# Kernel tuning notes

Hardware: AMD Instinct MI355X
Metric: run time of the kernel (lower is better)

## Reference

```python
import jax, jax.numpy as jnp
import numpy as np
from math import sqrt

B, S, E, H = 2, 2048, 768, 12
DH = E // H
W = 256            # one-sided attention window (attention_window=512)
G = 16             # number of global tokens (positions 0..G-1 in every batch row)
PAD = 128          # last PAD tokens per row are padding (masked)
FF = 3072          # SwiGLU intermediate size
NEG = -1e9
EPS = 1e-5


def _ln(x, g, b):
    m = jnp.mean(x, axis=-1, keepdims=True)
    v = jnp.var(x, axis=-1, keepdims=True)
    return (x - m) * jax.lax.rsqrt(v + EPS) * g + b


def _rope(x, t):
    # x: [B,H,S,DH]; t: [B,S] float 'set positions'
    half = DH // 2
    inv_freq = 1.0 / (10000.0 ** (jnp.arange(half, dtype=jnp.float32) / half))
    ang = t[:, None, :, None] * inv_freq            # [B,1,S,half]
    cos, sin = jnp.cos(ang), jnp.sin(ang)
    x1, x2 = x[..., :half], x[..., half:]
    return jnp.concatenate([x1 * cos - x2 * sin, x2 * cos + x1 * sin], axis=-1)


def _heads(x):  # [B,S,E] -> [B,H,S,DH]
    return x.reshape(B, S, H, DH).transpose(0, 2, 1, 3)


def _chunk3(x):
    # [B,H,S,D] -> [B,H,C,3W,D]: for query chunk c, keys from chunks c-1,c,c+1 (zero padded)
    b, h, s, d = x.shape
    c = s // W
    xp = jnp.pad(x, ((0, 0), (0, 0), (W, W), (0, 0))).reshape(b, h, c + 2, W, d)
    return jnp.concatenate([xp[:, :, :-2], xp[:, :, 1:-1], xp[:, :, 2:]], axis=3)


def _forward(x, attention_mask, global_attention_mask,
             Wq, bq, Wk, bk, Wv, bv, Wqg, bqg, Wkg, bkg, Wvg, bvg,
             ln0_g, ln0_b, ln1_g, ln1_b, W1, W3, W2):
    C = S // W
    merged = attention_mask * (global_attention_mask + 1)   # 0 masked, 1 local, 2 global
    is_masked = merged == 0
    is_global = merged == 2
    remove = merged != 1   # keys removed from windowed attention (masked or global)

    q = _heads(x @ Wq + bq) / sqrt(DH)
    k = _heads(x @ Wk + bk)
    v = _heads(x @ Wv + bv)

    # RoPE over 'set positions': (~is_index_masked) * cumsum(is_index_global_attn)
    t = jnp.where(is_masked, 0, jnp.cumsum(is_global.astype(jnp.int32), axis=1)).astype(jnp.float32)
    q = _rope(q, t)
    k = _rope(k, t)

    # --- sliding-window (banded) scores: band[b,h,i,d] = q_i . k_{i+d-W} ---
    qc = q.reshape(B, H, C, W, DH)
    k3 = _chunk3(k)
    s3 = jnp.einsum('bhcpd,bhcqd->bhcpq', qc, k3)                     # [B,H,C,W,3W]
    didx = jnp.arange(W)[:, None] + jnp.arange(2 * W + 1)[None, :]    # [W,2W+1]
    band = jnp.take_along_axis(s3, didx[None, None, None], axis=-1)   # [B,H,C,W,2W+1]

    # mask removed keys / out-of-range positions inside the band
    rmp = jnp.pad(remove, ((0, 0), (W, W)), constant_values=True).reshape(B, C + 2, W)
    rm3 = jnp.concatenate([rmp[:, :-2], rmp[:, 1:-1], rmp[:, 2:]], axis=2)  # [B,C,3W]
    band_rm = jnp.take_along_axis(jnp.broadcast_to(rm3[:, :, None, :], (B, C, W, 3 * W)),
                                  didx[None, None], axis=-1)                # [B,C,W,2W+1]
    band = jnp.where(band_rm[:, None], NEG, band).reshape(B, H, S, 2 * W + 1)

    # --- global-key columns (keys taken from the RoPE'd local key vectors) ---
    sg = jnp.einsum('bhid,bhgd->bhig', q, k[:, :, :G])                # [B,H,S,G]

    scores = jnp.concatenate([sg, band], axis=-1)                     # [B,H,S,G+2W+1]
    probs = jax.nn.softmax(scores.astype(jnp.float32), axis=-1).astype(x.dtype)
    probs = jnp.where(is_masked[:, None, :, None], 0.0, probs)

    # --- probs @ value: global columns + band ---
    out = jnp.einsum('bhig,bhgd->bhid', probs[..., :G], v[:, :, :G])
    pl = probs[..., G:].reshape(B, H, C, W, 2 * W + 1)
    rows = jnp.broadcast_to(jnp.arange(W)[:, None], (W, 2 * W + 1))
    p3 = jnp.zeros((B, H, C, W, 3 * W), probs.dtype).at[:, :, :, rows, didx].set(pl)
    v3 = _chunk3(v)
    out = out + jnp.einsum('bhcpq,bhcqd->bhcpd', p3, v3).reshape(B, H, S, DH)
    attn = out.transpose(0, 2, 1, 3).reshape(B, S, E)

    # --- full attention for global tokens (separate global projections, no RoPE) ---
    gq = _heads(x @ Wqg + bqg)[:, :, :G] / sqrt(DH)                   # [B,H,G,DH]
    gk = _heads(x @ Wkg + bkg)
    gv = _heads(x @ Wvg + bvg)
    gs = jnp.einsum('bhgd,bhjd->bhgj', gq, gk)                        # [B,H,G,S]
    gs = jnp.where(is_masked[:, None, None, :], NEG, gs)
    gp = jax.nn.softmax(gs.astype(jnp.float32), axis=-1).astype(x.dtype)
    gout = jnp.einsum('bhgj,bhjd->bhgd', gp, gv).transpose(0, 2, 1, 3).reshape(B, G, E)
    attn = attn.at[:, :G].set(gout)

    # residual + post-LN, SwiGLU FFN, residual + post-LN (dropout = eval mode)
    h0 = _ln(x + attn, ln0_g, ln0_b)
    ffn = (jax.nn.silu(h0 @ W1) * (h0 @ W3)) @ W2
    return _ln(h0 + ffn, ln1_g, ln1_b)


def setup_inputs():
    key = jax.random.key(0)
    ks = jax.random.split(key, 12)
    x = jax.random.normal(ks[0], (B, S, E), jnp.float32)
    attention_mask = jnp.ones((B, S), jnp.int32).at[:, S - PAD:].set(0)
    global_attention_mask = jnp.zeros((B, S), jnp.int32).at[:, :G].set(1)
    sd = 0.02
    def w(k, shape):
        return jax.random.normal(k, shape, jnp.float32) * sd
    return dict(
        x=x, attention_mask=attention_mask, global_attention_mask=global_attention_mask,
        Wq=w(ks[1], (E, E)), bq=jnp.zeros((E,), jnp.float32),
        Wk=w(ks[2], (E, E)), bk=jnp.zeros((E,), jnp.float32),
        Wv=w(ks[3], (E, E)), bv=jnp.zeros((E,), jnp.float32),
        Wqg=w(ks[4], (E, E)), bqg=jnp.zeros((E,), jnp.float32),
        Wkg=w(ks[5], (E, E)), bkg=jnp.zeros((E,), jnp.float32),
        Wvg=w(ks[6], (E, E)), bvg=jnp.zeros((E,), jnp.float32),
        ln0_g=jnp.ones((E,), jnp.float32), ln0_b=jnp.zeros((E,), jnp.float32),
        ln1_g=jnp.ones((E,), jnp.float32), ln1_b=jnp.zeros((E,), jnp.float32),
        W1=w(ks[7], (E, FF)), W3=w(ks[8], (E, FF)), W2=w(ks[9], (FF, E)))


def reference(x, attention_mask, global_attention_mask, Wq, bq, Wk, bk, Wv, bv,
              Wqg, bqg, Wkg, bkg, Wvg, bvg, ln0_g, ln0_b, ln1_g, ln1_b, W1, W3, W2):
    return _forward(x, attention_mask, global_attention_mask,
                    Wq, bq, Wk, bk, Wv, bv, Wqg, bqg, Wkg, bkg, Wvg, bvg,
                    ln0_g, ln0_b, ln1_g, ln1_b, W1, W3, W2)
```

## Files before the change

kernel.cpp:

```cpp
#include <hip/hip_runtime.h>


#define BB_ 2
#define SS 2048
#define EE 768
#define HH 12
#define DHH 64
#define GG 16
#define FFN 3072
#define MM (BB_*SS)

typedef __bf16 bf16_t;
typedef __bf16 bf16x8_t __attribute__((ext_vector_type(8)));
typedef float f32x4_t __attribute__((ext_vector_type(4)));

__device__ inline void gload16(const void* g, void* l) {
  __builtin_amdgcn_global_load_lds((const __attribute__((address_space(1))) void*)g,
                                   (__attribute__((address_space(3))) void*)l, 16, 0, 0);
}

__global__ __launch_bounds__(64) void detect_kernel(const unsigned int* __restrict__ w,
                                                    int* __restrict__ flag) {
  int cnt = 0;
  for (int i = threadIdx.x; i < 1024; i += 64) {
    unsigned e = (w[i] >> 7) & 0xFF;
    cnt += (e >= 100 && e <= 144) ? 1 : 0;
  }
  for (int off = 32; off; off >>= 1) cnt += __shfl_xor(cnt, off);
  if (threadIdx.x == 0) flag[0] = (cnt > 512) ? 1 : 0;
}

struct CanonP { const void* src[11]; bf16_t* dst[11]; };

__global__ __launch_bounds__(256) void canon_kernel(CanonP P, const int* __restrict__ flag) {
  constexpr int ns[11] = {3145728, 768,768,768,768,768,768, 768,768,768,768};
  int idx4 = (blockIdx.x*256 + threadIdx.x)*4;
  const bool isb = flag[0] != 0;
  int off = 0, seg = -1, loc = 0;
  #pragma unroll
  for (int i=0;i<11;i++) {
    if (seg < 0 && idx4 < off + ns[i]) { seg = i; loc = idx4 - off; }
    off += ns[i];
  }
  if (seg < 0) return;
  const void* s = P.src[seg];
  bf16_t* d = P.dst[seg];
  if (isb) {
    *(uint2*)&d[loc] = *(const uint2*)((const unsigned short*)s + loc);
  } else {
    float4 v = *(const float4*)((const float*)s + loc);
    d[loc+0] = (bf16_t)v.x; d[loc+1] = (bf16_t)v.y;
    d[loc+2] = (bf16_t)v.z; d[loc+3] = (bf16_t)v.w;
  }
}

struct TP6 { const void* s[6]; bf16_t* d[6]; };

__global__ __launch_bounds__(256) void trans_kernel(TP6 P, int R, int C,
                                                    const int* __restrict__ flag) {
  const int z = blockIdx.z;
  const void* src = P.s[z]; bf16_t* dst = P.d[z];
  const bool isb = flag[0] != 0;
  __shared__ bf16_t tile[32][33];
  int tx = threadIdx.x & 31, ty = threadIdx.x >> 5;
  int r0 = blockIdx.y*32, c0 = blockIdx.x*32;
  #pragma unroll
  for (int i=0;i<4;i++) {
    int rr = ty + i*8;
    size_t si = (size_t)(r0+rr)*C + c0 + tx;
    tile[rr][tx] = isb ? ((const bf16_t*)src)[si] : (bf16_t)((const float*)src)[si];
  }
  __syncthreads();
  #pragma unroll
  for (int i=0;i<4;i++) {
    int cc = ty + i*8;
    dst[(size_t)(c0+cc)*R + r0 + tx] = tile[tx][cc];
  }
}

__global__ __launch_bounds__(256) void zero_kernel(float* __restrict__ p, int n) {
  int i = blockIdx.x*256 + threadIdx.x;
  if (i < n) p[i] = 0.f;
}

__global__ __launch_bounds__(256) void flags_kernel(const int* __restrict__ am,
                                                    const int* __restrict__ gm,
                                                    float* __restrict__ tpos,
                                                    int* __restrict__ flags) {
  int b = blockIdx.x;
  int t = threadIdx.x;
  int lane = t & 63, wv = t >> 6;
  int base = b*SS + t*8;
  int mg[8]; int isg[8]; int loc = 0;
  for (int i=0;i<8;i++) {
    int a = am[base+i], g = gm[base+i];
    int merged = a*(g+1);
    mg[i] = merged;
    isg[i] = (merged==2) ? 1 : 0;
    loc += isg[i];
  }
  int x = loc;
  for (int off=1; off<64; off<<=1) {
    int y = __shfl_up(x, off);
    if (lane >= off) x += y;
  }
  __shared__ int wtot[4];
  if (lane==63) wtot[wv] = x;
  __syncthreads();
  int prev = 0;
  for (int w=0; w<wv; w++) prev += wtot[w];
  int run = prev + x - loc;
  for (int i=0;i<8;i++) {
    run += isg[i];
    int masked = (mg[i]==0) ? 1 : 0;
    int glob   = (mg[i]==2) ? 1 : 0;
    int rem    = (mg[i]!=1) ? 1 : 0;
    tpos[base+i]  = masked ? 0.f : (float)run;
    flags[base+i] = masked | (glob<<1) | (rem<<2);
  }
}

__device__ inline void gemm128_core(const bf16_t* __restrict__ A,
                                    const bf16_t* __restrict__ BT,
                                    int ldA, int ldB, int kbeg, int kend,
                                    int m0, int n0,
                                    bf16_t* As, bf16_t* Bs,
                                    f32x4_t (&acc)[4][4]) {
  const int t = threadIdx.x;
  const int lane = t & 63, wv = t >> 6;
  const int l15 = lane & 15, quad = lane >> 4;
  const int wr = (wv >> 1) << 6, wc = (wv & 1) << 6;
  const int rsub = lane >> 3, pch = lane & 7;
  const int sch = pch ^ rsub;
  const size_t abase = (size_t)(m0 + wv*32 + rsub)*ldA + sch*8;
  const size_t bbase = (size_t)(n0 + wv*32 + rsub)*ldB + sch*8;
  const int sx = l15 & 7;
  bf16_t* lA = As + (wv*32)*64;
  bf16_t* lB = Bs + (wv*32)*64;
  for (int k0 = kbeg; k0 < kend; k0 += 64) {
    __syncthreads();
    #pragma unroll
    for (int j=0;j<4;j++) {
      gload16(A + abase + (size_t)(j*8)*ldA + k0, lA + j*8*64);
      gload16(BT + bbase + (size_t)(j*8)*ldB + k0, lB + j*8*64);
    }
    __syncthreads();
    #pragma unroll
    for (int c=0;c<2;c++) {
      bf16x8_t af[4], bfr[4];
      #pragma unroll
      for (int a=0;a<4;a++)
        af[a] = *(const bf16x8_t*)&As[(wr + a*16 + l15)*64 + ((c*4+quad)^sx)*8];
      #pragma unroll
      for (int b=0;b<4;b++)
        bfr[b] = *(const bf16x8_t*)&Bs[(wc + b*16 + l15)*64 + ((c*4+quad)^sx)*8];
      #pragma unroll
      for (int a=0;a<4;a++)
        #pragma unroll
        for (int b=0;b<4;b++)
          acc[a][b] = __builtin_amdgcn_mfma_f32_16x16x32_bf16(af[a], bfr[b], acc[a][b], 0,0,0);
    }
  }
}

struct ProjParams {
  const bf16_t* W[5];
  const bf16_t* Bi[5];
  bf16_t* O[5];
};

__global__ __launch_bounds__(256) void proj_kernel(const bf16_t* __restrict__ x,
                                                   ProjParams P,
                                                   const float* __restrict__ tpos) {
  const int m0 = blockIdx.x*128, n0 = blockIdx.y*128;
  const int z  = blockIdx.z;
  __shared__ bf16_t As[128*64];
  __shared__ bf16_t Bs[128*64];
  f32x4_t acc[4][4];
  #pragma unroll
  for (int a=0;a<4;a++)
    #pragma unroll
    for (int b=0;b<4;b++) acc[a][b] = (f32x4_t){0.f,0.f,0.f,0.f};
  gemm128_core(x, P.W[z], EE, EE, 0, EE, m0, n0, As, Bs, acc);

  const int t = threadIdx.x;
  const int lane = t & 63, wv = t >> 6;
  const int l15 = lane & 15, quad = lane >> 4;
  const int wr = (wv >> 1) << 6, wc = (wv & 1) << 6;
  const float scale = (z==0) ? 0.125f : 1.f;
  const bool rope = (z<2);
  const int h = (n0 + wc) >> 6;
  bf16_t* Oz = P.O[z];
  const bf16_t* Bz = P.Bi[z];
  float bvals[4];
  #pragma unroll
  for (int b=0;b<4;b++) bvals[b] = (float)Bz[h*64 + b*16 + l15];
  #pragma unroll
  for (int a=0;a<4;a++) {
    #pragma unroll
    for (int r=0;r<4;r++) {
      int row = m0 + wr + a*16 + quad*4 + r;
      int bb = row >> 11, spos = row & (SS-1);
      float vals[4];
      #pragma unroll
      for (int b=0;b<4;b++) vals[b] = (acc[a][b][r] + bvals[b]) * scale;
      if (rope) {
        float tv = tpos[row];
        #pragma unroll
        for (int b=0;b<2;b++) {
          int j = b*16 + l15;
          float inv = __expf(-(float)j * (9.210340371976184f/32.f));
          float ang = tv * inv;
          float sn = __sinf(ang), cs = __cosf(ang);
          float x1 = vals[b], x2 = vals[b+2];
          vals[b]   = x1*cs - x2*sn;
          vals[b+2] = x2*cs + x1*sn;
        }
      }
      bf16_t* dst = Oz + ((size_t)(bb*HH + h)*SS + spos)*DHH;
      #pragma unroll
      for (int b=0;b<4;b++) dst[b*16 + l15] = (bf16_t)vals[b];
    }
  }
}

__global__ __launch_bounds__(256) void gemm_ffn1(const bf16_t* __restrict__ A,
                                                 const bf16_t* __restrict__ BT,
                                                 bf16_t* __restrict__ t1) {
  const int m0 = blockIdx.x*128, n0 = blockIdx.y*128;
  __shared__ bf16_t As[128*64];
  __shared__ bf16_t Bs[128*64];
  f32x4_t acc[4][4];
  #pragma unroll
  for (int a=0;a<4;a++)
    #pragma unroll
    for (int b=0;b<4;b++) acc[a][b] = (f32x4_t){0.f,0.f,0.f,0.f};
  gemm128_core(A, BT, EE, EE, 0, EE, m0, n0, As, Bs, acc);
  const int t = threadIdx.x;
  const int lane = t & 63, wv = t >> 6;
  const int l15 = lane & 15, quad = lane >> 4;
  const int wr = (wv >> 1) << 6, wc = (wv & 1) << 6;
  #pragma unroll
  for (int a=0;a<4;a++)
    #pragma unroll
    for (int r=0;r<4;r++) {
      int row = m0 + wr + a*16 + quad*4 + r;
      #pragma unroll
      for (int b=0;b<4;b++)
        t1[(size_t)row*FFN + n0 + wc + b*16 + l15] = (bf16_t)acc[a][b][r];
    }
}

__global__ __launch_bounds__(256) void gemm_ffn3(const bf16_t* __restrict__ A,
                                                 const bf16_t* __restrict__ BT,
                                                 const bf16_t* __restrict__ t1,
                                                 bf16_t* __restrict__ g1) {
  const int m0 = blockIdx.x*128, n0 = blockIdx.y*128;
  __shared__ bf16_t As[128*64];
  __shared__ bf16_t Bs[128*64];
  f32x4_t acc[4][4];
  #pragma unroll
  for (int a=0;a<4;a++)
    #pragma unroll
    for (int b=0;b<4;b++) acc[a][b] = (f32x4_t){0.f,0.f,0.f,0.f};
  gemm128_core(A, BT, EE, EE, 0, EE, m0, n0, As, Bs, acc);
  const int t = threadIdx.x;
  const int lane = t & 63, wv = t >> 6;
  const int l15 = lane & 15, quad = lane >> 4;
  const int wr = (wv >> 1) << 6, wc = (wv & 1) << 6;
  #pragma unroll
  for (int a=0;a<4;a++)
    #pragma unroll
    for (int r=0;r<4;r++) {
      int row = m0 + wr + a*16 + quad*4 + r;
      #pragma unroll
      for (int b=0;b<4;b++) {
        size_t idx = (size_t)row*FFN + n0 + wc + b*16 + l15;
        float a1 = (float)t1[idx];
        float sil = a1 / (1.f + __expf(-a1));
        g1[idx] = (bf16_t)(sil * acc[a][b][r]);
      }
    }
}

struct Ffn2Out { float* p[4]; };

__global__ __launch_bounds__(256) void gemm_ffn2(const bf16_t* __restrict__ A,
                                                 const bf16_t* __restrict__ BT,
                                                 Ffn2Out O) {
  const int m0 = blockIdx.x*128, n0 = blockIdx.y*128;
  const int kz = blockIdx.z;
  __shared__ bf16_t As[128*64];
  __shared__ bf16_t Bs[128*64];
  f32x4_t acc[4][4];
  #pragma unroll
  for (int a=0;a<4;a++)
    #pragma unroll
    for (int b=0;b<4;b++) acc[a][b] = (f32x4_t){0.f,0.f,0.f,0.f};
  gemm128_core(A, BT, FFN, FFN, kz*768, (kz+1)*768, m0, n0, As, Bs, acc);
  const int t = threadIdx.x;
  const int lane = t & 63, wv = t >> 6;
  const int l15 = lane & 15, quad = lane >> 4;
  const int wr = (wv >> 1) << 6, wc = (wv & 1) << 6;
  float* C = O.p[kz];
  #pragma unroll
  for (int a=0;a<4;a++)
    #pragma unroll
    for (int r=0;r<4;r++) {
      int row = m0 + wr + a*16 + quad*4 + r;
      #pragma unroll
      for (int b=0;b<4;b++)
        C[(size_t)row*EE + n0 + wc + b*16 + l15] = acc[a][b][r];
    }
}

__global__ __launch_bounds__(64) void qg_kernel(const bf16_t* __restrict__ x,
                                                const bf16_t* __restrict__ WqgT,
                                                const bf16_t* __restrict__ bqg,
                                                float* __restrict__ qgb) {
  int g = blockIdx.x, h = blockIdx.y, b = blockIdx.z;
  int d = threadIdx.x;
  __shared__ float xs[EE];
  for (int i=d; i<EE; i+=64) xs[i] = (float)x[((size_t)b*SS + g)*EE + i];
  __syncthreads();
  float acc = 0.f;
  const bf16_t* wrow = WqgT + (size_t)(h*64+d)*EE;
  #pragma unroll 4
  for (int k=0;k<EE;k+=8) {
    bf16x8_t w8 = *(const bf16x8_t*)(wrow + k);
    #pragma unroll
    for (int i=0;i<8;i++) acc += xs[k+i] * (float)w8[i];
  }
  acc = (acc + (float)bqg[h*64+d]) * 0.125f;
  qgb[((size_t)(b*HH+h)*GG + g)*DHH + d] = acc;
}

__global__ __launch_bounds__(256) void band_kernel(const bf16_t* __restrict__ qb,
                                                   const bf16_t* __restrict__ kb,
                                                   const bf16_t* __restrict__ vb,
                                                   const int* __restrict__ flags,
                                                   float* __restrict__ attn) {
  const int p0 = blockIdx.x*64;
  const int h = blockIdx.y, b = blockIdx.z;
  const int t = threadIdx.x;
  const int wv = t>>6, lane = t&63;
  const int l15 = lane & 15, quad = lane >> 4;
  const size_t bh = (size_t)(b*HH+h);
  const bf16_t* kbh = kb + bh*SS*DHH;
  const bf16_t* vbh = vb + bh*SS*DHH;
  const int* fl = flags + b*SS;
  const int q0 = p0 + wv*16;

  __shared__ bf16_t Vt[64*72];
  __shared__ bf16_t Pw[4][16*72];

  const bf16_t* qrow = qb + (bh*SS + q0 + l15)*DHH;
  bf16x8_t qa0 = *(const bf16x8_t*)(qrow + quad*8);
  bf16x8_t qa1 = *(const bf16x8_t*)(qrow + 32 + quad*8);

  f32x4_t o[4];
  #pragma unroll
  for (int i=0;i<4;i++) o[i] = (f32x4_t){0.f,0.f,0.f,0.f};
  float lsum[4] = {0.f,0.f,0.f,0.f};
  bf16_t* P = Pw[wv];

  for (int unit=0; unit<10; unit++) {
    const int kb0 = (unit<9) ? (p0 - 256 + unit*64) : 0;
    __syncthreads();
    {
      int kp  = (t & 31)*2;
      int dh0 = (t >> 5)*8;
      int k1 = kb0 + kp, k2 = kb0 + kp + 1;
      int kc1 = min(max(k1,0),SS-1), kc2 = min(max(k2,0),SS-1);
      bf16x8_t v1 = *(const bf16x8_t*)(vbh + (size_t)kc1*DHH + dh0);
      bf16x8_t v2 = *(const bf16x8_t*)(vbh + (size_t)kc2*DHH + dh0);
      #pragma unroll
      for (int i=0;i<8;i++) {
        union { unsigned u; bf16_t hh[2]; } pk;
        pk.hh[0] = v1[i]; pk.hh[1] = v2[i];
        *(unsigned*)&Vt[(dh0+i)*72 + kp] = pk.u;
      }
    }
    __syncthreads();
    const int nsub = (unit<9) ? 4 : 1;
    for (int sub=0; sub<4; sub++) {
      if (sub < nsub) {
        int kpos = kb0 + sub*16 + l15;
        int kc = min(max(kpos,0),SS-1);
        const bf16_t* krow = kbh + (size_t)kc*DHH;
        bf16x8_t kf0 = *(const bf16x8_t*)(krow + quad*8);
        bf16x8_t kf1 = *(const bf16x8_t*)(krow + 32 + quad*8);
        f32x4_t s = (f32x4_t){0.f,0.f,0.f,0.f};
        s = __builtin_amdgcn_mfma_f32_16x16x32_bf16(qa0, kf0, s, 0,0,0);
        s = __builtin_amdgcn_mfma_f32_16x16x32_bf16(qa1, kf1, s, 0,0,0);
        bool drop = false;
        if (unit<9) drop = (kpos<0) || (kpos>=SS) || (((fl[kc]>>2)&1)!=0);
        #pragma unroll
        for (int r=0;r<4;r++) {
          float e;
          if (unit==9) {
            e = __expf(s[r]);
          } else {
            int dj = kpos - (q0 + quad*4 + r);
            bool valid = (dj>=-256) && (dj<=256) && (!drop);
            e = valid ? __expf(s[r]) : 0.f;
          }
          lsum[r] += e;
          P[(quad*4+r)*72 + sub*16 + l15] = (bf16_t)e;
        }
      } else {
        #pragma unroll
        for (int r=0;r<4;r++) P[(quad*4+r)*72 + sub*16 + l15] = (bf16_t)0.f;
      }
    }
    #pragma unroll
    for (int chunk=0; chunk<2; chunk++) {
      bf16x8_t pf = *(const bf16x8_t*)&P[l15*72 + chunk*32 + quad*8];
      #pragma unroll
      for (int nt=0; nt<4; nt++) {
        bf16x8_t vf = *(const bf16x8_t*)&Vt[(nt*16+l15)*72 + chunk*32 + quad*8];
        o[nt] = __builtin_amdgcn_mfma_f32_16x16x32_bf16(pf, vf, o[nt], 0,0,0);
      }
    }
  }
  #pragma unroll
  for (int r=0;r<4;r++) {
    float s = lsum[r];
    s += __shfl_xor(s,1); s += __shfl_xor(s,2);
    s += __shfl_xor(s,4); s += __shfl_xor(s,8);
    lsum[r] = s;
  }
  #pragma unroll
  for (int r=0;r<4;r++) {
    int q = q0 + quad*4 + r;
    int masked = fl[q] & 1;
    float inv = masked ? 0.f : 1.f/lsum[r];
    float* dst = attn + ((size_t)(b*SS+q))*EE + h*64 + l15;
    #pragma unroll
    for (int nt=0; nt<4; nt++) dst[nt*16] = o[nt][r]*inv;
  }
}

__global__ __launch_bounds__(256) void gattn_part(const float* __restrict__ qgb,
                                                  const bf16_t* __restrict__ kgb,
                                                  const bf16_t* __restrict__ vgb,
                                                  const int* __restrict__ flags,
                                                  float* __restrict__ go,
                                                  float* __restrict__ gl) {
  const int kbase = blockIdx.x*128;
  const int h = blockIdx.y, b = blockIdx.z;
  const int t = threadIdx.x;
  __shared__ float gqs[16*68];
  __shared__ float Ks[64*68];
  __shared__ float Vs[64*68];
  __shared__ float es[16*64];
  const size_t bh = (size_t)(b*HH+h);
  #pragma unroll
  for (int j=0;j<4;j++) {
    int idx = t + j*256;
    int g = idx>>6, d = idx&63;
    gqs[g*68+d] = qgb[(bh*GG + g)*DHH + d];
  }
  float accv[4] = {0.f,0.f,0.f,0.f};
  float lpart = 0.f;
  const int gs = t>>4, kslot = t&15;
  const int dp = t&63, grp = t>>6;
  const bf16_t* kb_ = kgb + bh*SS*DHH;
  const bf16_t* vb_ = vgb + bh*SS*DHH;
  const int* fl = flags + b*SS;
  for (int tile=0; tile<2; tile++) {
    int k0 = kbase + tile*64;
    __syncthreads();
    {
      int row = t>>2, seg = t&3;
      const bf16_t* sk = kb_ + (size_t)(k0+row)*DHH + seg*16;
      const bf16_t* sv = vb_ + (size_t)(k0+row)*DHH + seg*16;
      bf16x8_t k1 = *(const bf16x8_t*)sk;
      bf16x8_t k2 = *(const bf16x8_t*)(sk+8);
      bf16x8_t v1 = *(const bf16x8_t*)sv;
      bf16x8_t v2 = *(const bf16x8_t*)(sv+8);
      #pragma unroll
      for (int i=0;i<8;i++) {
        Ks[row*68 + seg*16 + i]     = (float)k1[i];
        Ks[row*68 + seg*16 + 8 + i] = (float)k2[i];
        Vs[row*68 + seg*16 + i]     = (float)v1[i];
        Vs[row*68 + seg*16 + 8 + i] = (float)v2[i];
      }
    }
    __syncthreads();
    #pragma unroll
    for (int j=0;j<4;j++) {
      int key = kslot + 16*j;
      const float* gq = &gqs[gs*68];
      const float* kr = &Ks[key*68];
      float s = 0.f;
      #pragma unroll
      for (int d4=0; d4<64; d4+=4) {
        float4 a = *(const float4*)(gq + d4);
        float4 kk = *(const float4*)(kr + d4);
        s += a.x*kk.x + a.y*kk.y + a.z*kk.z + a.w*kk.w;
      }
      int msk = fl[k0+key] & 1;
      float e = msk ? 0.f : __expf(s);
      es[gs*64+key] = e;
      lpart += e;
    }
    __syncthreads();
    #pragma unroll
    for (int g=0; g<4; g++) {
      int gg = grp*4+g;
      float a = accv[g];
      for (int key=0;key<64;key++) a += es[gg*64+key]*Vs[key*68+dp];
      accv[g] = a;
    }
  }
  __syncthreads();
  es[gs*64 + kslot] = lpart;
  __syncthreads();
  if (t < 16) {
    float s = 0.f;
    for (int j=0;j<16;j++) s += es[t*64+j];
    atomicAdd(&gl[bh*16 + t], s);
  }
  #pragma unroll
  for (int g=0; g<4; g++)
    atomicAdd(&go[(bh*16 + grp*4+g)*64 + dp], accv[g]);
}

__global__ __launch_bounds__(256) void addln_kernel(const bf16_t* __restrict__ Abf,
                                                    const float* __restrict__ Af,
                                                    const float* __restrict__ B0,
                                                    const float* __restrict__ B1,
                                                    const float* __restrict__ B2,
                                                    const float* __restrict__ B3,
                                                    const float* __restrict__ gof,
                                                    const float* __restrict__ glf,
                                                    const bf16_t* __restrict__ gw,
                                                    const bf16_t* __restrict__ bw,
                                                    float* __restrict__ outf,
                                                    bf16_t* __restrict__ outb,
                                                    const int* __restrict__ flagp) {
  int r = blockIdx.x, t = threadIdx.x;
  int lane = t&63, wv = t>>6;
  int spos = r & (SS-1), bb = r >> 11;
  bool isglob = (gof != nullptr) && (spos < GG);
  float v[3]; float sum=0.f, ss=0.f;
  #pragma unroll
  for (int j=0;j<3;j++) {
    int idx = t + j*256;
    size_t gi = (size_t)r*EE+idx;
    float a = Abf ? (float)Abf[gi] : Af[gi];
    float bv;
    if (isglob) {
      int hh = idx >> 6, dp = idx & 63;
      int slot = (bb*HH + hh)*GG + spos;
      bv = gof[(size_t)slot*DHH + dp] / glf[slot];
    } else {
      bv = B0[gi];
    }
    float val = a + bv;
    if (B1) val += B1[gi] + B2[gi] + B3[gi];
    v[j] = val; sum += val; ss += val*val;
  }
  #pragma unroll
  for (int off=32; off>=1; off>>=1) {
    sum += __shfl_xor(sum, off);
    ss  += __shfl_xor(ss, off);
  }
  __shared__ float s1[4], s2[4];
  if (lane==0) { s1[wv]=sum; s2[wv]=ss; }
  __syncthreads();
  sum = s1[0]+s1[1]+s1[2]+s1[3];
  ss  = s2[0]+s2[1]+s2[2]+s2[3];
  float mean = sum * (1.f/(float)EE);
  float var  = ss * (1.f/(float)EE) - mean*mean;
  float rstd = rsqrtf(var + 1e-5f);
  bool wantb, wantf;
  if (flagp) { bool isb = (*flagp)!=0; wantb = isb; wantf = !isb; }
  else { wantb = (outb!=nullptr); wantf = (outf!=nullptr); }
  #pragma unroll
  for (int j=0;j<3;j++) {
    int idx = t + j*256;
    float o = (v[j]-mean)*rstd*(float)gw[idx] + (float)bw[idx];
    if (wantf) outf[(size_t)r*EE+idx] = o;
    if (wantb) outb[(size_t)r*EE+idx] = (bf16_t)o;
  }
}

extern "C" void kernel_launch(void* const* d_in, const int* in_sizes, int n_in,
                              void* d_out, int out_size, void* d_ws, size_t ws_size,
                              hipStream_t stream) {
  const void* x_r    = d_in[0];
  const int* am      = (const int*)d_in[1];
  const int* gm      = (const int*)d_in[2];
  (void)in_sizes; (void)n_in; (void)out_size; (void)ws_size;

  char* ws = (char*)d_ws;
  size_t off = 0;
  auto alloc = [&](size_t bytes) -> void* {
    void* p = ws + off;
    off += (bytes + 255) & ~(size_t)255;
    return p;
  };
  bf16_t* xc    = (bf16_t*)alloc((size_t)MM*EE*2);
  bf16_t* WT[6]; bf16_t* bc[6];
  for (int i=0;i<6;i++) { WT[i] = (bf16_t*)alloc((size_t)EE*EE*2); bc[i] = (bf16_t*)alloc(EE*2); }
  bf16_t* lnc[4];
  for (int i=0;i<4;i++) lnc[i] = (bf16_t*)alloc(EE*2);
  bf16_t* W1T = (bf16_t*)alloc((size_t)EE*FFN*2);
  bf16_t* W3T = (bf16_t*)alloc((size_t)EE*FFN*2);
  bf16_t* W2T = (bf16_t*)alloc((size_t)FFN*EE*2);
  const size_t NBHSD = (size_t)BB_*HH*SS*DHH;
  bf16_t* qb    = (bf16_t*)alloc(NBHSD*2);
  bf16_t* kb    = (bf16_t*)alloc(NBHSD*2);
  bf16_t* vb    = (bf16_t*)alloc(NBHSD*2);
  bf16_t* kgb   = (bf16_t*)alloc(NBHSD*2);
  bf16_t* vgb   = (bf16_t*)alloc(NBHSD*2);
  float* qgb   = (float*)alloc((size_t)BB_*HH*GG*DHH*4);
  float* attn  = (float*)alloc((size_t)MM*EE*4);
  float* h0f   = (float*)alloc((size_t)MM*EE*4);
  bf16_t* h0b  = (bf16_t*)alloc((size_t)MM*EE*2);
  bf16_t* g1   = (bf16_t*)alloc((size_t)MM*FFN*2);
  float* p3    = (float*)alloc((size_t)MM*EE*4);
  float* go    = (float*)alloc((size_t)BB_*HH*GG*DHH*4);
  float* gl    = (float*)alloc((size_t)BB_*HH*GG*4);
  float* tposb = (float*)alloc((size_t)BB_*SS*4);
  int*   flagb = (int*)alloc((size_t)BB_*SS*4);
  int*   dflag = (int*)alloc(256);
  bf16_t* t1 = qb;
  float* p1 = (float*)qb;
  float* p2 = (float*)qb + (size_t)MM*EE;

  detect_kernel<<<1, 64, 0, stream>>>((const unsigned int*)d_in[3], dflag);

  CanonP CP;
  const void* csrc[11] = { x_r, d_in[4], d_in[6], d_in[8], d_in[10], d_in[12], d_in[14],
                           d_in[15], d_in[16], d_in[17], d_in[18] };
  bf16_t* cdst[11] = { xc, bc[0], bc[1], bc[2], bc[3], bc[4], bc[5],
                       lnc[0], lnc[1], lnc[2], lnc[3] };
  for (int i=0;i<11;i++) { CP.src[i]=csrc[i]; CP.dst[i]=cdst[i]; }
  canon_kernel<<<3081, 256, 0, stream>>>(CP, dflag);

  TP6 T6;
  const int wi[6] = {3,5,7,9,11,13};
  for (int i=0;i<6;i++) { T6.s[i]=d_in[wi[i]]; T6.d[i]=WT[i]; }
  trans_kernel<<<dim3(24,24,6), 256, 0, stream>>>(T6, EE, EE, dflag);
  TP6 TF; TF.s[0]=d_in[19]; TF.d[0]=W1T; TF.s[1]=d_in[20]; TF.d[1]=W3T;
  for (int i=2;i<6;i++) { TF.s[i]=d_in[19]; TF.d[i]=W1T; }
  trans_kernel<<<dim3(96,24,2), 256, 0, stream>>>(TF, EE, FFN, dflag);
  TP6 T2; T2.s[0]=d_in[21]; T2.d[0]=W2T;
  for (int i=1;i<6;i++) { T2.s[i]=d_in[21]; T2.d[i]=W2T; }
  trans_kernel<<<dim3(24,96,1), 256, 0, stream>>>(T2, FFN, EE, dflag);

  zero_kernel<<<98, 256, 0, stream>>>(go, 24960);

  flags_kernel<<<BB_, 256, 0, stream>>>(am, gm, tposb, flagb);

  ProjParams P;
  P.W[0]=WT[0]; P.Bi[0]=bc[0]; P.O[0]=qb;
  P.W[1]=WT[1]; P.Bi[1]=bc[1]; P.O[1]=kb;
  P.W[2]=WT[2]; P.Bi[2]=bc[2]; P.O[2]=vb;
  P.W[3]=WT[4]; P.Bi[3]=bc[4]; P.O[3]=kgb;
  P.W[4]=WT[5]; P.Bi[4]=bc[5]; P.O[4]=vgb;
  proj_kernel<<<dim3(MM/128, EE/128, 5), 256, 0, stream>>>(xc, P, tposb);

  qg_kernel<<<dim3(GG, HH, BB_), 64, 0, stream>>>(xc, WT[3], bc[3], qgb);

  band_kernel<<<dim3(SS/64, HH, BB_), 256, 0, stream>>>(qb, kb, vb, flagb, attn);

  gattn_part<<<dim3(SS/128, HH, BB_), 256, 0, stream>>>(qgb, kgb, vgb, flagb, go, gl);

  addln_kernel<<<MM, 256, 0, stream>>>(xc, nullptr, attn, nullptr, nullptr, nullptr,
                                       go, gl, lnc[0], lnc[1], h0f, h0b, nullptr);

  gemm_ffn1<<<dim3(MM/128, FFN/128), 256, 0, stream>>>(h0b, W1T, t1);
  gemm_ffn3<<<dim3(MM/128, FFN/128), 256, 0, stream>>>(h0b, W3T, t1, g1);
  Ffn2Out FO; FO.p[0]=attn; FO.p[1]=p1; FO.p[2]=p2; FO.p[3]=p3;
  gemm_ffn2<<<dim3(MM/128, EE/128, 4), 256, 0, stream>>>(g1, W2T, FO);

  addln_kernel<<<MM, 256, 0, stream>>>(nullptr, h0f, attn, p1, p2, p3,
                                       nullptr, nullptr, lnc[2], lnc[3],
                                       (float*)d_out, (bf16_t*)d_out, dflag);
}
```

Measured before the change: 388.0 us.

## Double-buffer K/V tiles in LDS for band attention with swizzled K loads

The banded attention kernel now stages K tiles in LDS through async global-to-LDS loads into an XOR-swizzled layout, and double-buffers both K and transposed V so the next unit's loads overlap the current unit's MFMA work. This removes one barrier per unit and avoids re-reading K rows from global memory in each wave. The grid is flattened and remapped so that consecutive blocks are spread across the eight XCDs, and s_setprio raises priority around the PV MFMAs. It costs more LDS per block, which may lower occupancy, and depends on the new barrier placement to keep the two buffers from racing.

New measurement: 364.2 us. 1.07x faster.

```diff
diff --git a/kernel.cpp b/kernel.cpp
--- a/kernel.cpp
+++ b/kernel.cpp
@@ -340,8 +340,13 @@
                                                    const bf16_t* __restrict__ vb,
                                                    const int* __restrict__ flags,
                                                    float* __restrict__ attn) {
-  const int p0 = blockIdx.x*64;
-  const int h = blockIdx.y, b = blockIdx.z;
+  const int flat = blockIdx.x;
+  const int nb = (flat & 7) * 96 + (flat >> 3);
+  const int px = nb & 31;
+  const int hb = nb >> 5;
+  const int h = hb % HH, b = hb / HH;
+  const int p0 = px * 64;
+
   const int t = threadIdx.x;
   const int wv = t>>6, lane = t&63;
   const int l15 = lane & 15, quad = lane >> 4;
@@ -351,13 +356,39 @@
   const int* fl = flags + b*SS;
   const int q0 = p0 + wv*16;
 
-  __shared__ bf16_t Vt[64*72];
+  __shared__ bf16_t Ks[2][64*DHH];
+  __shared__ bf16_t Vt[2][64*72];
   __shared__ bf16_t Pw[4][16*72];
 
   const bf16_t* qrow = qb + (bh*SS + q0 + l15)*DHH;
   bf16x8_t qa0 = *(const bf16x8_t*)(qrow + quad*8);
   bf16x8_t qa1 = *(const bf16x8_t*)(qrow + 32 + quad*8);
 
+  const int srsub = lane >> 3, spch = lane & 7;
+  const int vkp  = (t & 31) * 2;
+  const int vdh0 = (t >> 5) * 8;
+
+  {
+    const int kb0 = p0 - 256;
+    #pragma unroll
+    for (int j=0;j<2;j++) {
+      int row = wv*16 + j*8 + srsub;
+      int kc = min(max(kb0 + row, 0), SS-1);
+      gload16(kbh + (size_t)kc*DHH + (spch ^ srsub)*8, &Ks[0][(wv*16 + j*8)*DHH]);
+    }
+    int kc1 = min(max(kb0 + vkp,   0), SS-1);
+    int kc2 = min(max(kb0 + vkp+1, 0), SS-1);
+    bf16x8_t v1 = *(const bf16x8_t*)(vbh + (size_t)kc1*DHH + vdh0);
+    bf16x8_t v2 = *(const bf16x8_t*)(vbh + (size_t)kc2*DHH + vdh0);
+    #pragma unroll
+    for (int i=0;i<8;i++) {
+      union { unsigned u; bf16_t hh[2]; } pk;
+      pk.hh[0] = v1[i]; pk.hh[1] = v2[i];
+      *(unsigned*)&Vt[0][(vdh0+i)*72 + vkp] = pk.u;
+    }
+  }
+  __syncthreads();
+
   f32x4_t o[4];
   #pragma unroll
   for (int i=0;i<4;i++) o[i] = (f32x4_t){0.f,0.f,0.f,0.f};
@@ -365,34 +396,35 @@
   bf16_t* P = Pw[wv];
 
   for (int unit=0; unit<10; unit++) {
+    const int cur = unit & 1, nxt = cur ^ 1;
     const int kb0 = (unit<9) ? (p0 - 256 + unit*64) : 0;
-    __syncthreads();
-    {
-      int kp  = (t & 31)*2;
-      int dh0 = (t >> 5)*8;
-      int k1 = kb0 + kp, k2 = kb0 + kp + 1;
-      int kc1 = min(max(k1,0),SS-1), kc2 = min(max(k2,0),SS-1);
-      bf16x8_t v1 = *(const bf16x8_t*)(vbh + (size_t)kc1*DHH + dh0);
-      bf16x8_t v2 = *(const bf16x8_t*)(vbh + (size_t)kc2*DHH + dh0);
-      #pragma unroll
-      for (int i=0;i<8;i++) {
-        union { unsigned u; bf16_t hh[2]; } pk;
-        pk.hh[0] = v1[i]; pk.hh[1] = v2[i];
-        *(unsigned*)&Vt[(dh0+i)*72 + kp] = pk.u;
+    const bool pre = (unit < 9);
+    bf16x8_t pv1, pv2;
+    if (pre) {
+      const int kbn = (unit < 8) ? (kb0 + 64) : 0;
+      #pragma unroll
+      for (int j=0;j<2;j++) {
+        int row = wv*16 + j*8 + srsub;
+        int kc = min(max(kbn + row, 0), SS-1);
+        gload16(kbh + (size_t)kc*DHH + (spch ^ srsub)*8, &Ks[nxt][(wv*16 + j*8)*DHH]);
       }
-    }
-    __syncthreads();
+      int kc1 = min(max(kbn + vkp,   0), SS-1);
+      int kc2 = min(max(kbn + vkp+1, 0), SS-1);
+      pv1 = *(const bf16x8_t*)(vbh + (size_t)kc1*DHH + vdh0);
+      pv2 = *(const bf16x8_t*)(vbh + (size_t)kc2*DHH + vdh0);
+    }
+    const bf16_t* Kc = Ks[cur];
     const int nsub = (unit<9) ? 4 : 1;
     for (int sub=0; sub<4; sub++) {
       if (sub < nsub) {
-        int kpos = kb0 + sub*16 + l15;
-        int kc = min(max(kpos,0),SS-1);
-        const bf16_t* krow = kbh + (size_t)kc*DHH;
-        bf16x8_t kf0 = *(const bf16x8_t*)(krow + quad*8);
-        bf16x8_t kf1 = *(const bf16x8_t*)(krow + 32 + quad*8);
+        int krow = sub*16 + l15;
+        int kpos = kb0 + krow;
+        bf16x8_t kf0 = *(const bf16x8_t*)&Kc[krow*DHH + (((quad  ) ^ (krow&7))<<3)];
+        bf16x8_t kf1 = *(const bf16x8_t*)&Kc[krow*DHH + (((quad+4) ^ (krow&7))<<3)];
         f32x4_t s = (f32x4_t){0.f,0.f,0.f,0.f};
         s = __builtin_amdgcn_mfma_f32_16x16x32_bf16(qa0, kf0, s, 0,0,0);
         s = __builtin_amdgcn_mfma_f32_16x16x32_bf16(qa1, kf1, s, 0,0,0);
+        int kc = min(max(kpos,0),SS-1);
         bool drop = false;
         if (unit<9) drop = (kpos<0) || (kpos>=SS) || (((fl[kc]>>2)&1)!=0);
         #pragma unroll
@@ -413,14 +445,25 @@
         for (int r=0;r<4;r++) P[(quad*4+r)*72 + sub*16 + l15] = (bf16_t)0.f;
       }
     }
+    __builtin_amdgcn_s_setprio(1);
     #pragma unroll
     for (int chunk=0; chunk<2; chunk++) {
       bf16x8_t pf = *(const bf16x8_t*)&P[l15*72 + chunk*32 + quad*8];
       #pragma unroll
       for (int nt=0; nt<4; nt++) {
-        bf16x8_t vf = *(const bf16x8_t*)&Vt[(nt*16+l15)*72 + chunk*32 + quad*8];
+        bf16x8_t vf = *(const bf16x8_t*)&Vt[cur][(nt*16+l15)*72 + chunk*32 + quad*8];
         o[nt] = __builtin_amdgcn_mfma_f32_16x16x32_bf16(pf, vf, o[nt], 0,0,0);
       }
+    }
+    __builtin_amdgcn_s_setprio(0);
+    if (pre) {
+      #pragma unroll
+      for (int i=0;i<8;i++) {
+        union { unsigned u; bf16_t hh[2]; } pk;
+        pk.hh[0] = pv1[i]; pk.hh[1] = pv2[i];
+        *(unsigned*)&Vt[nxt][(vdh0+i)*72 + vkp] = pk.u;
+      }
+      __syncthreads();
     }
   }
   #pragma unroll
@@ -666,7 +709,7 @@
 
   qg_kernel<<<dim3(GG, HH, BB_), 64, 0, stream>>>(xc, WT[3], bc[3], qgb);
 
-  band_kernel<<<dim3(SS/64, HH, BB_), 256, 0, stream>>>(qb, kb, vb, flagb, attn);
+  band_kernel<<<dim3(768), 256, 0, stream>>>(qb, kb, vb, flagb, attn);
 
   gattn_part<<<dim3(SS/128, HH, BB_), 256, 0, stream>>>(qgb, kgb, vgb, flagb, go, gl);
 
```
